# Optimization experiments

Hardware: AMD Instinct MI355X
Metric: run time of the kernel (lower is better)

The kernel has to match this reference:

```python
import jax, jax.numpy as jnp
import numpy as np

BSZ, SEQ, HID = 4, 2048, 2048
NH, NKV, HD = 16, 8, 128
SLOTS, MAXSEQ = 8, 4096
EPS = 1e-6
SCALE = HD ** -0.5


def rms_norm(x, w):
    # normalize over last dim (head_dim)
    var = jnp.mean(jnp.square(x), axis=-1, keepdims=True)
    return x * jax.lax.rsqrt(var + EPS) * w


def setup_inputs() -> dict:
    key = jax.random.key(0)
    ks = jax.random.split(key, 6)
    return {
        "hidden_states": jax.random.normal(ks[0], (BSZ, SEQ, HID), jnp.float32),
        "positions": jnp.tile(jnp.arange(SEQ, dtype=jnp.int32)[None, :], (BSZ, 1)),
        "k_cache": jnp.zeros((SLOTS, MAXSEQ, NKV, HD), jnp.float32),
        "v_cache": jnp.zeros((SLOTS, MAXSEQ, NKV, HD), jnp.float32),
        "slot_mapping": jnp.arange(BSZ, dtype=jnp.int32),
        "kv_start_indices": jnp.zeros((BSZ,), jnp.int32),
        "seq_lens": jnp.full((BSZ,), SEQ, jnp.int32),
        "qkv_w": jax.random.normal(ks[1], ((NH + 2 * NKV) * HD, HID), jnp.float32) * 0.02,
        "qkv_b": jax.random.normal(ks[2], ((NH + 2 * NKV) * HD,), jnp.float32) * 0.02,
        "o_w": jax.random.normal(ks[3], (HID, NH * HD), jnp.float32) * 0.02,
        "q_norm_w": jnp.ones((HD,), jnp.float32),
        "k_norm_w": jnp.ones((HD,), jnp.float32),
    }


def reference(hidden_states, positions, k_cache, v_cache, slot_mapping,
              kv_start_indices, seq_lens, qkv_w, qkv_b, o_w, q_norm_w, k_norm_w):
    bsz, seq_len, _ = hidden_states.shape
    qkv = jnp.einsum("bsh,oh->bso", hidden_states, qkv_w) + qkv_b
    q, k, v = jnp.split(qkv, [NH * HD, NH * HD + NKV * HD], axis=-1)
    q = rms_norm(q.reshape(bsz, seq_len, NH, HD), q_norm_w)
    k = rms_norm(k.reshape(bsz, seq_len, NKV, HD), k_norm_w)
    v = v.reshape(bsz, seq_len, NKV, HD)

    # paged KV cache scatter: cache[slot, start:start+seq] = k/v  (vectorized over batch)
    rows = kv_start_indices[:, None] + jnp.arange(seq_len)[None, :]  # [B,S]
    k_cache = k_cache.at[slot_mapping[:, None], rows].set(k)
    v_cache = v_cache.at[slot_mapping[:, None], rows].set(v)

    # prefill path (seq_len > 1): gather back up to max_l (= seq_len here, static)
    max_l = seq_len
    k_h = k_cache[slot_mapping, :max_l].transpose(0, 2, 1, 3)  # [B,Hkv,L,D]
    v_h = v_cache[slot_mapping, :max_l].transpose(0, 2, 1, 3)
    n_rep = NH // NKV
    if n_rep > 1:  # repeat_interleave over head dim (GQA)
        k_h = jnp.repeat(k_h, n_rep, axis=1)
        v_h = jnp.repeat(v_h, n_rep, axis=1)

    qh = q.transpose(0, 2, 1, 3)  # [B,H,S,D]
    scores = jnp.einsum("bhqd,bhkd->bhqk", qh, k_h) * SCALE
    causal = jnp.tril(jnp.ones((seq_len, max_l), bool))
    scores = jnp.where(causal[None, None], scores, -jnp.inf)
    attn = jax.nn.softmax(scores, axis=-1)
    out = jnp.einsum("bhqk,bhkd->bhqd", attn, v_h)
    out = out.transpose(0, 2, 1, 3).reshape(bsz, seq_len, NH * HD)
    return jnp.einsum("bso,ho->bsh", out, o_w)
```

## Files before the change

kernel.cpp:

```cpp
#include <hip/hip_runtime.h>
#include <hip/hip_bf16.h>
#include <stdint.h>

typedef unsigned short u16;
typedef __attribute__((ext_vector_type(8))) __bf16 bf16x8;
typedef __attribute__((ext_vector_type(4))) float f32x4;

#define EPSF 1e-6f
#define SCALE 0.08838834764831845f

__device__ __forceinline__ u16 f2bf(float f) {
    union { float f; uint32_t u; } a; a.f = f;
    uint32_t r = a.u + 0x7FFFu + ((a.u >> 16) & 1u);
    return (u16)(r >> 16);
}
__device__ __forceinline__ float bf2f(u16 u) {
    union { uint32_t u; float f; } a; a.u = ((uint32_t)u) << 16;
    return a.f;
}
__device__ __forceinline__ u16 f2bf_n(float f) {
    __hip_bfloat16 h = __float2bfloat16(f);
    return *reinterpret_cast<u16*>(&h);
}

__global__ __launch_bounds__(256) void cvt_all_k(
    const float* __restrict__ a,
    const float* __restrict__ b,
    const float* __restrict__ c,
    u16* __restrict__ out)
{
    long i = (long)blockIdx.x * 256 + threadIdx.x;
    const float* src; long off;
    if (i < 4194304L)      { src = a; off = 0; }
    else if (i < 6291456L) { src = b; off = 4194304L; }
    else                   { src = c; off = 6291456L; }
    float4 v = ((const float4*)src)[i - off];
    ushort4 o;
    o.x = f2bf(v.x); o.y = f2bf(v.y); o.z = f2bf(v.z); o.w = f2bf(v.w);
    ((ushort4*)out)[i] = o;
}

__device__ __forceinline__ void gload16(const u16* g, u16* l) {
    __builtin_amdgcn_global_load_lds(
        (const __attribute__((address_space(1))) uint32_t*)g,
        (__attribute__((address_space(3))) uint32_t*)l, 16, 0, 0);
}

__global__ __launch_bounds__(512, 2) void gemm8_nt(
    const u16* __restrict__ A, const u16* __restrict__ B,
    const float* __restrict__ bias,
    float* __restrict__ Cf, u16* __restrict__ Cb,
    int M, int N, int K)
{
    __shared__ u16 As[2][256 * 64];
    __shared__ u16 Bs[2][256 * 64];

    const int t = threadIdx.x;
    const int lane = t & 63;
    const int g = lane >> 4, lr = lane & 15;
    const int w = t >> 6;
    const int wm = w >> 2, wn = w & 3;

    const int nwg = gridDim.x * gridDim.y;
    const int bid0 = blockIdx.y * gridDim.x + blockIdx.x;
    const int cpx = nwg >> 3;
    const int bids = (bid0 & 7) * cpx + (bid0 >> 3);
    const int bn = (bids % gridDim.x) * 256;
    const int bm = (bids / gridDim.x) * 256;
    const int NT = K >> 6;

    f32x4 z = {0.f, 0.f, 0.f, 0.f};
    f32x4 acc[8][4];
#pragma unroll
    for (int m = 0; m < 8; ++m)
#pragma unroll
        for (int n = 0; n < 4; ++n) acc[m][n] = z;

    auto STAGE2 = [&](int buf, int k0, int p) {
#pragma unroll
        for (int j = 0; j < 2; ++j) {
            int idx = p * 1024 + j * 512 + t;
            int ci = idx & 2047;
            int row = ci >> 3, slot = ci & 7;
            int csrc = slot ^ (row & 7);
            if (idx < 2048)
                gload16(A + (size_t)(bm + row) * K + k0 + csrc * 8, &As[buf][0] + ci * 8);
            else
                gload16(B + (size_t)(bn + row) * K + k0 + csrc * 8, &Bs[buf][0] + ci * 8);
        }
    };

    bf16x8 afr0[4][2], afr1[4][2];
    bf16x8 bf0[2][2], bf1[2][2];

#pragma unroll
    for (int p = 0; p < 4; ++p) STAGE2(0, 0, p);

    for (int kt = 0; kt < NT; ++kt) {
        const int cur = kt & 1;
        const int k0n = (kt + 1) << 6;
        const bool last = (kt == NT - 1);
        const char* Ab = (const char*)&As[cur][0];
        const char* Bb = (const char*)&Bs[cur][0];
        const int swz = (lr & 7) << 4;

        auto LDA = [&](bf16x8 (&dst)[4][2], int mbase) {
#pragma unroll
            for (int mi = 0; mi < 4; ++mi) {
                int row = wm * 128 + (mbase + mi) * 16 + lr;
#pragma unroll
                for (int kc = 0; kc < 2; ++kc)
                    dst[mi][kc] = *(const bf16x8*)(Ab + row * 128 + ((kc * 64 + g * 16) ^ swz));
            }
        };
        auto LDB = [&](bf16x8 (&dst)[2][2], int nbase) {
#pragma unroll
            for (int ni = 0; ni < 2; ++ni) {
                int row = wn * 64 + (nbase + ni) * 16 + lr;
#pragma unroll
                for (int kc = 0; kc < 2; ++kc)
                    dst[ni][kc] = *(const bf16x8*)(Bb + row * 128 + ((kc * 64 + g * 16) ^ swz));
            }
        };
        auto MMA = [&](bf16x8 (&amf)[4][2], int mf0, int nf0, bf16x8 (&bfr)[2][2]) {
            __builtin_amdgcn_s_setprio(1);
#pragma unroll
            for (int mi = 0; mi < 4; ++mi)
#pragma unroll
                for (int ni = 0; ni < 2; ++ni)
#pragma unroll
                    for (int kc = 0; kc < 2; ++kc)
                        acc[mf0 + mi][nf0 + ni] = __builtin_amdgcn_mfma_f32_16x16x32_bf16(
                            amf[mi][kc], bfr[ni][kc], acc[mf0 + mi][nf0 + ni], 0, 0, 0);
            __builtin_amdgcn_s_setprio(0);
        };

        if (!last) {
#pragma unroll
            for (int p = 0; p < 4; ++p) STAGE2(cur ^ 1, k0n, p);
            asm volatile("s_waitcnt vmcnt(8)" ::: "memory");
        } else {
            asm volatile("s_waitcnt vmcnt(0)" ::: "memory");
        }
        __builtin_amdgcn_s_barrier();
        __builtin_amdgcn_sched_barrier(0);

        LDA(afr0, 0); LDB(bf0, 0); LDB(bf1, 2);
        MMA(afr0, 0, 0, bf0);
        MMA(afr0, 0, 2, bf1);
        LDA(afr1, 4);
        MMA(afr1, 4, 2, bf1);
        MMA(afr1, 4, 0, bf0);

        __builtin_amdgcn_sched_barrier(0);
        __builtin_amdgcn_s_barrier();
    }

#pragma unroll
    for (int mf = 0; mf < 8; ++mf) {
#pragma unroll
        for (int nf = 0; nf < 4; ++nf) {
            int col = bn + wn * 64 + nf * 16 + lr;
            float bv = bias ? bias[col] : 0.f;
#pragma unroll
            for (int r = 0; r < 4; ++r) {
                int row = bm + wm * 128 + mf * 16 + g * 4 + r;
                float v = acc[mf][nf][r] + bv;
                if (Cf) Cf[(size_t)row * N + col] = v;
                else    Cb[(size_t)row * N + col] = f2bf(v);
            }
        }
    }
}

__global__ __launch_bounds__(256) void prep_k(
    u16* __restrict__ qkv, const float* __restrict__ qw, const float* __restrict__ kw,
    u16* __restrict__ vt)
{
    __shared__ u16 T[64 * 64];
    const int bid = blockIdx.x;
    const int t = threadIdx.x;

    if (bid < 8192) {
        const int row = bid;
        const int w = t >> 6, l = t & 63;
#pragma unroll
        for (int i = 0; i < 6; ++i) {
            int head = w + i * 4;
            const float* wt = (head < 16) ? qw : kw;
            u16* p = qkv + (size_t)row * 4096 + head * 128;
            uint32_t u = *(const uint32_t*)(p + l * 2);
            float x0 = bf2f((u16)(u & 0xFFFF));
            float x1 = bf2f((u16)(u >> 16));
            float ss = x0 * x0 + x1 * x1;
#pragma unroll
            for (int m = 1; m < 64; m <<= 1) ss += __shfl_xor(ss, m, 64);
            float inv = rsqrtf(ss * (1.0f / 128.0f) + EPSF);
            float r0 = x0 * inv * wt[l * 2];
            float r1 = x1 * inv * wt[l * 2 + 1];
            uint32_t o = (uint32_t)f2bf(r0) | ((uint32_t)f2bf(r1) << 16);
            *(uint32_t*)(p + l * 2) = o;
        }
    } else {
        const int q = bid - 8192;
        const int sx = (q & 31) * 64;
        const int dy = ((q >> 5) & 1) * 64;
        const int z  = q >> 6;
        const int b = z >> 3, hk = z & 7;
#pragma unroll
        for (int j = 0; j < 2; ++j) {
            int idx = t + j * 256;
            int r = idx >> 3, c8 = (idx & 7) * 8;
            uint4 v = *(const uint4*)(qkv + (size_t)(b * 2048 + sx + r) * 4096 + 3072 + hk * 128 + dy + c8);
            int slot = (c8 >> 3) ^ ((r ^ (r >> 3)) & 7);
            *(uint4*)(&T[r * 64 + slot * 8]) = v;
        }
        __syncthreads();
#pragma unroll
        for (int j = 0; j < 2; ++j) {
            int idx = t + j * 256;
            int rr = idx >> 3, cc8 = (idx & 7) * 8;
            u16 tmp[8];
#pragma unroll
            for (int i = 0; i < 8; ++i) {
                int row = cc8 + i;
                int slot = (rr >> 3) ^ ((row ^ (row >> 3)) & 7);
                tmp[i] = T[row * 64 + slot * 8 + (rr & 7)];
            }
            *(uint4*)(vt + ((size_t)z * 128 + dy + rr) * 2048 + sx + cc8) = *(uint4*)tmp;
        }
    }
}

#define P_S 72

__global__ __launch_bounds__(256, 2) void attn5_k(
    const u16* __restrict__ qkv, const u16* __restrict__ vt,
    u16* __restrict__ aout)
{
    __shared__ u16 Kt[2][64 * 128];
    __shared__ u16 Vl[2][128 * 64];
    __shared__ u16 P[4][16 * P_S];

    const int t = threadIdx.x;
    const int lane = t & 63;
    const int w = t >> 6;
    const int g = lane >> 4, lr = lane & 15;
    const int pr = blockIdx.x, h = blockIdx.y, b = blockIdx.z;
    const int hk = h >> 1;
    const size_t rowb = (size_t)b * 2048;

    const u16* ksrc = qkv + rowb * 4096 + 2048 + hk * 128;
    const u16* vsrc = vt + (size_t)(b * 8 + hk) * 128 * 2048;

    bf16x8 ones8;
    {
        union { bf16x8 v; u16 e[8]; } on;
#pragma unroll
        for (int j = 0; j < 8; ++j) on.e[j] = 0x3F80;
        ones8 = on.v;
    }

    auto STAGE = [&](int buf, int kvb) {
#pragma unroll
        for (int j = 0; j < 4; ++j) {
            int idx = t + j * 256;
            {
                int row = idx >> 4, slot = idx & 15;
                int csrc = (slot & 8) | ((slot & 7) ^ (row & 7));
                gload16(ksrc + (size_t)(kvb + row) * 4096 + csrc * 8, &Kt[buf][0] + idx * 8);
            }
            {
                int row = idx >> 3, slot = idx & 7;
                int csrc = slot ^ (row & 7);
                gload16(vsrc + (size_t)row * 2048 + kvb + csrc * 8, &Vl[buf][0] + idx * 8);
            }
        }
    };

    for (int sub = 0; sub < 2; ++sub) {
        const int qt = sub ? 15 - pr : pr;
        const int qbase = qt * 128;
        const int nt = 2 * qt + 2;

        bf16x8 qf[2][4];
        {
            const u16* qp = qkv + (rowb + qbase + w * 32 + lr) * 4096 + h * 128;
#pragma unroll
            for (int sb = 0; sb < 2; ++sb)
#pragma unroll
                for (int c = 0; c < 4; ++c) {
                    union { bf16x8 v; u16 e[8]; } uq;
                    uq.v = *(const bf16x8*)(qp + sb * 16 * 4096 + c * 32 + g * 8);
#pragma unroll
                    for (int jj = 0; jj < 8; ++jj) uq.e[jj] = f2bf(bf2f(uq.e[jj]) * SCALE);
                    qf[sb][c] = uq.v;
                }
        }

        float m_r[2][4];
        f32x4 z = {0.f, 0.f, 0.f, 0.f};
        f32x4 l_acc[2];
        f32x4 o_acc[2][8];
#pragma unroll
        for (int sb = 0; sb < 2; ++sb) {
#pragma unroll
            for (int r = 0; r < 4; ++r) m_r[sb][r] = -INFINITY;
            l_acc[sb] = z;
#pragma unroll
            for (int d = 0; d < 8; ++d) o_acc[sb][d] = z;
        }

        __syncthreads();
        STAGE(0, 0);

        for (int kt = 0; kt < nt; ++kt) {
            const int cur = kt & 1;
            const int kvb = kt * 64;
            asm volatile("s_waitcnt vmcnt(0)" ::: "memory");
            __builtin_amdgcn_s_barrier();
            __builtin_amdgcn_sched_barrier(0);
            if (kt + 1 < nt) STAGE(cur ^ 1, kvb + 64);
            __builtin_amdgcn_sched_barrier(0);

            const u16* Kc = &Kt[cur][0];
            const u16* Vc = &Vl[cur][0];
            const bool active = !(kt == nt - 1 && w < 2);
            const bool near = (kt >= nt - 2);

            if (active) {
                f32x4 s[2][4];
                __builtin_amdgcn_s_setprio(1);
#pragma unroll
                for (int cb = 0; cb < 4; ++cb) {
                    int row = cb * 16 + lr;
                    s[0][cb] = z; s[1][cb] = z;
#pragma unroll
                    for (int c = 0; c < 4; ++c) {
                        int chunk = c * 4 + g;
                        int slot = (chunk & 8) | ((chunk & 7) ^ (row & 7));
                        bf16x8 kf = *(const bf16x8*)(&Kc[row * 128 + slot * 8]);
                        s[0][cb] = __builtin_amdgcn_mfma_f32_16x16x32_bf16(qf[0][c], kf, s[0][cb], 0, 0, 0);
                        s[1][cb] = __builtin_amdgcn_mfma_f32_16x16x32_bf16(qf[1][c], kf, s[1][cb], 0, 0, 0);
                    }
                }
                __builtin_amdgcn_s_setprio(0);

#pragma unroll
                for (int sb = 0; sb < 2; ++sb) {
#pragma unroll
                    for (int r = 0; r < 4; ++r) {
                        float v0 = s[sb][0][r], v1 = s[sb][1][r], v2 = s[sb][2][r], v3 = s[sb][3][r];
                        if (near) {
                            int qa = qbase + w * 32 + sb * 16 + g * 4 + r;
                            if (kvb + lr > qa)      v0 = -INFINITY;
                            if (kvb + 16 + lr > qa) v1 = -INFINITY;
                            if (kvb + 32 + lr > qa) v2 = -INFINITY;
                            if (kvb + 48 + lr > qa) v3 = -INFINITY;
                        }
                        float mx = fmaxf(fmaxf(v0, v1), fmaxf(v2, v3));
                        mx = fmaxf(mx, __shfl_xor(mx, 1));
                        mx = fmaxf(mx, __shfl_xor(mx, 2));
                        mx = fmaxf(mx, __shfl_xor(mx, 4));
                        mx = fmaxf(mx, __shfl_xor(mx, 8));
                        float mold = m_r[sb][r];
                        float mbase;
                        if (__all(mx <= mold + 8.0f)) {
                            mbase = mold;
                        } else {
                            float mnew = fmaxf(mold, mx);
                            float alpha = __expf(mold - mnew);
                            l_acc[sb][r] *= alpha;
#pragma unroll
                            for (int d = 0; d < 8; ++d) o_acc[sb][d][r] *= alpha;
                            m_r[sb][r] = mnew;
                            mbase = mnew;
                        }
                        float p0 = __expf(v0 - mbase), p1 = __expf(v1 - mbase);
                        float p2 = __expf(v2 - mbase), p3 = __expf(v3 - mbase);
                        int prow = (g * 4 + r) * P_S;
                        P[w][prow + lr]      = f2bf_n(p0);
                        P[w][prow + 16 + lr] = f2bf_n(p1);
                        P[w][prow + 32 + lr] = f2bf_n(p2);
                        P[w][prow + 48 + lr] = f2bf_n(p3);
                    }

#pragma unroll
                    for (int kk = 0; kk < 2; ++kk) {
                        bf16x8 pa = *(const bf16x8*)(&P[w][lr * P_S + kk * 32 + g * 8]);
                        __builtin_amdgcn_s_setprio(1);
                        l_acc[sb] = __builtin_amdgcn_mfma_f32_16x16x32_bf16(pa, ones8, l_acc[sb], 0, 0, 0);
#pragma unroll
                        for (int d = 0; d < 8; ++d) {
                            int row = d * 16 + lr;
                            int slot = (kk * 4 + g) ^ (row & 7);
                            bf16x8 vf = *(const bf16x8*)(&Vc[row * 64 + slot * 8]);
                            o_acc[sb][d] = __builtin_amdgcn_mfma_f32_16x16x32_bf16(pa, vf, o_acc[sb][d], 0, 0, 0);
                        }
                        __builtin_amdgcn_s_setprio(0);
                    }
                }
            }
            __builtin_amdgcn_sched_barrier(0);
        }

#pragma unroll
        for (int sb = 0; sb < 2; ++sb) {
            const int qrow0 = qbase + w * 32 + sb * 16 + g * 4;
#pragma unroll
            for (int r = 0; r < 4; ++r) {
                float inv = 1.0f / l_acc[sb][r];
                u16* op = aout + (rowb + qrow0 + r) * 2048 + h * 128;
#pragma unroll
                for (int d = 0; d < 8; ++d)
                    op[d * 16 + lr] = f2bf_n(o_acc[sb][d][r] * inv);
            }
        }
    }
}

extern "C" void kernel_launch(void* const* d_in, const int* in_sizes, int n_in,
                              void* d_out, int out_size, void* d_ws, size_t ws_size,
                              hipStream_t stream)
{
    const float* hidden = (const float*)d_in[0];
    const float* qkv_w = (const float*)d_in[7];
    const float* qkv_b = (const float*)d_in[8];
    const float* o_w   = (const float*)d_in[9];
    const float* q_nw  = (const float*)d_in[10];
    const float* k_nw  = (const float*)d_in[11];

    char* ws = (char*)d_ws;
    u16* hid_bf  = (u16*)ws; ws += (size_t)8192 * 2048 * 2;
    u16* wqkv_bf = (u16*)ws; ws += (size_t)4096 * 2048 * 2;
    u16* ow_bf   = (u16*)ws; ws += (size_t)2048 * 2048 * 2;
    u16* qkv_bf  = (u16*)ws; ws += (size_t)8192 * 4096 * 2;
    u16* attn_bf = (u16*)ws; ws += (size_t)8192 * 2048 * 2;
    u16* vt_bf   = hid_bf;

    cvt_all_k<<<28672, 256, 0, stream>>>(hidden, qkv_w, o_w, hid_bf);

    gemm8_nt<<<dim3(16, 32), 512, 0, stream>>>(hid_bf, wqkv_bf, qkv_b,
                                               nullptr, qkv_bf, 8192, 4096, 2048);
    prep_k<<<dim3(10240), 256, 0, stream>>>(qkv_bf, q_nw, k_nw, vt_bf);
    attn5_k<<<dim3(8, 16, 4), 256, 0, stream>>>(qkv_bf, vt_bf, attn_bf);
    gemm8_nt<<<dim3(8, 32), 512, 0, stream>>>(attn_bf, ow_bf, nullptr,
                                              (float*)d_out, nullptr, 8192, 2048, 2048);
}
```

Measured before the change: 404.1 us.

## Compute transposed scores and pass softmax probabilities via lane shuffles instead of LDS

The QK^T MFMA operands are swapped, so each lane holds score columns for a single query row. The row max then needs only two cross-lane shuffles, and each lane keeps one running max per row block instead of four. Probabilities are packed to bf16 in registers and redistributed into the PV MFMA operand layout with __shfl, which removes the per-wave LDS P buffer and its store/load round trip. In exchange the kernel issues more ds_bpermute shuffles and select instructions, and rescaling needs an extra shuffle to broadcast alpha to each row.

Result: faster. 378.1 us (median of 2 runs) (-6.4%).

```diff
diff --git a/kernel.cpp b/kernel.cpp
--- a/kernel.cpp
+++ b/kernel.cpp
@@ -232,15 +232,12 @@
     }
 }
 
-#define P_S 72
-
-__global__ __launch_bounds__(256, 2) void attn5_k(
+__global__ __launch_bounds__(256, 2) void attn7_k(
     const u16* __restrict__ qkv, const u16* __restrict__ vt,
     u16* __restrict__ aout)
 {
     __shared__ u16 Kt[2][64 * 128];
     __shared__ u16 Vl[2][128 * 64];
-    __shared__ u16 P[4][16 * P_S];
 
     const int t = threadIdx.x;
     const int lane = t & 63;
@@ -298,14 +295,13 @@
                 }
         }
 
-        float m_r[2][4];
+        float m_r2[2];
         f32x4 z = {0.f, 0.f, 0.f, 0.f};
         f32x4 l_acc[2];
         f32x4 o_acc[2][8];
 #pragma unroll
         for (int sb = 0; sb < 2; ++sb) {
-#pragma unroll
-            for (int r = 0; r < 4; ++r) m_r[sb][r] = -INFINITY;
+            m_r2[sb] = -INFINITY;
             l_acc[sb] = z;
 #pragma unroll
             for (int d = 0; d < 8; ++d) o_acc[sb][d] = z;
@@ -329,73 +325,96 @@
             const bool near = (kt >= nt - 2);
 
             if (active) {
-                f32x4 s[2][4];
+                f32x4 st[2][4];
                 __builtin_amdgcn_s_setprio(1);
 #pragma unroll
                 for (int cb = 0; cb < 4; ++cb) {
                     int row = cb * 16 + lr;
-                    s[0][cb] = z; s[1][cb] = z;
+                    st[0][cb] = z; st[1][cb] = z;
 #pragma unroll
                     for (int c = 0; c < 4; ++c) {
                         int chunk = c * 4 + g;
                         int slot = (chunk & 8) | ((chunk & 7) ^ (row & 7));
                         bf16x8 kf = *(const bf16x8*)(&Kc[row * 128 + slot * 8]);
-                        s[0][cb] = __builtin_amdgcn_mfma_f32_16x16x32_bf16(qf[0][c], kf, s[0][cb], 0, 0, 0);
-                        s[1][cb] = __builtin_amdgcn_mfma_f32_16x16x32_bf16(qf[1][c], kf, s[1][cb], 0, 0, 0);
+                        st[0][cb] = __builtin_amdgcn_mfma_f32_16x16x32_bf16(kf, qf[0][c], st[0][cb], 0, 0, 0);
+                        st[1][cb] = __builtin_amdgcn_mfma_f32_16x16x32_bf16(kf, qf[1][c], st[1][cb], 0, 0, 0);
                     }
                 }
                 __builtin_amdgcn_s_setprio(0);
 
+                const int slo = ((g & 1) << 5) + lr;
+                const int shi = slo + 16;
+                const bool ghx = (g >> 1) & 1;
+
 #pragma unroll
                 for (int sb = 0; sb < 2; ++sb) {
-#pragma unroll
-                    for (int r = 0; r < 4; ++r) {
-                        float v0 = s[sb][0][r], v1 = s[sb][1][r], v2 = s[sb][2][r], v3 = s[sb][3][r];
-                        if (near) {
-                            int qa = qbase + w * 32 + sb * 16 + g * 4 + r;
-                            if (kvb + lr > qa)      v0 = -INFINITY;
-                            if (kvb + 16 + lr > qa) v1 = -INFINITY;
-                            if (kvb + 32 + lr > qa) v2 = -INFINITY;
-                            if (kvb + 48 + lr > qa) v3 = -INFINITY;
+                    const int qa = qbase + w * 32 + sb * 16 + lr;
+                    if (near) {
+#pragma unroll
+                        for (int cb = 0; cb < 4; ++cb)
+#pragma unroll
+                            for (int r = 0; r < 4; ++r)
+                                if (kvb + cb * 16 + g * 4 + r > qa) st[sb][cb][r] = -INFINITY;
+                    }
+                    f32x4 m4;
+#pragma unroll
+                    for (int e = 0; e < 4; ++e)
+                        m4[e] = fmaxf(fmaxf(st[sb][0][e], st[sb][1][e]),
+                                      fmaxf(st[sb][2][e], st[sb][3][e]));
+                    float mx = fmaxf(fmaxf(m4[0], m4[1]), fmaxf(m4[2], m4[3]));
+                    mx = fmaxf(mx, __shfl_xor(mx, 16));
+                    mx = fmaxf(mx, __shfl_xor(mx, 32));
+                    float mold = m_r2[sb];
+                    float mbase;
+                    if (__all(mx <= mold + 8.0f)) {
+                        mbase = mold;
+                    } else {
+                        float mnew = fmaxf(mold, mx);
+                        float alpha = __expf(mold - mnew);
+#pragma unroll
+                        for (int r = 0; r < 4; ++r) {
+                            float ar = __shfl(alpha, (lane & 48) | (g * 4 + r), 64);
+                            l_acc[sb][r] *= ar;
+#pragma unroll
+                            for (int d = 0; d < 8; ++d) o_acc[sb][d][r] *= ar;
                         }
-                        float mx = fmaxf(fmaxf(v0, v1), fmaxf(v2, v3));
-                        mx = fmaxf(mx, __shfl_xor(mx, 1));
-                        mx = fmaxf(mx, __shfl_xor(mx, 2));
-                        mx = fmaxf(mx, __shfl_xor(mx, 4));
-                        mx = fmaxf(mx, __shfl_xor(mx, 8));
-                        float mold = m_r[sb][r];
-                        float mbase;
-                        if (__all(mx <= mold + 8.0f)) {
-                            mbase = mold;
-                        } else {
-                            float mnew = fmaxf(mold, mx);
-                            float alpha = __expf(mold - mnew);
-                            l_acc[sb][r] *= alpha;
-#pragma unroll
-                            for (int d = 0; d < 8; ++d) o_acc[sb][d][r] *= alpha;
-                            m_r[sb][r] = mnew;
-                            mbase = mnew;
-                        }
-                        float p0 = __expf(v0 - mbase), p1 = __expf(v1 - mbase);
-                        float p2 = __expf(v2 - mbase), p3 = __expf(v3 - mbase);
-                        int prow = (g * 4 + r) * P_S;
-                        P[w][prow + lr]      = f2bf_n(p0);
-                        P[w][prow + 16 + lr] = f2bf_n(p1);
-                        P[w][prow + 32 + lr] = f2bf_n(p2);
-                        P[w][prow + 48 + lr] = f2bf_n(p3);
+                        m_r2[sb] = mnew;
+                        mbase = mnew;
                     }
+                    uint2 pk[4];
+#pragma unroll
+                    for (int cb = 0; cb < 4; ++cb) {
+                        float p0 = __expf(st[sb][cb][0] - mbase);
+                        float p1 = __expf(st[sb][cb][1] - mbase);
+                        float p2 = __expf(st[sb][cb][2] - mbase);
+                        float p3 = __expf(st[sb][cb][3] - mbase);
+                        pk[cb].x = (uint32_t)f2bf_n(p0) | ((uint32_t)f2bf_n(p1) << 16);
+                        pk[cb].y = (uint32_t)f2bf_n(p2) | ((uint32_t)f2bf_n(p3) << 16);
+                    }
 
 #pragma unroll
                     for (int kk = 0; kk < 2; ++kk) {
-                        bf16x8 pa = *(const bf16x8*)(&P[w][lr * P_S + kk * 32 + g * 8]);
+                        uint32_t e0 = (uint32_t)__shfl((int)pk[kk * 2].x, slo, 64);
+                        uint32_t e1 = (uint32_t)__shfl((int)pk[kk * 2].y, slo, 64);
+                        uint32_t e2 = (uint32_t)__shfl((int)pk[kk * 2].x, shi, 64);
+                        uint32_t e3 = (uint32_t)__shfl((int)pk[kk * 2].y, shi, 64);
+                        uint32_t o0 = (uint32_t)__shfl((int)pk[kk * 2 + 1].x, slo, 64);
+                        uint32_t o1 = (uint32_t)__shfl((int)pk[kk * 2 + 1].y, slo, 64);
+                        uint32_t o2 = (uint32_t)__shfl((int)pk[kk * 2 + 1].x, shi, 64);
+                        uint32_t o3 = (uint32_t)__shfl((int)pk[kk * 2 + 1].y, shi, 64);
+                        union { uint32_t u[4]; bf16x8 v; } pa;
+                        pa.u[0] = ghx ? o0 : e0;
+                        pa.u[1] = ghx ? o1 : e1;
+                        pa.u[2] = ghx ? o2 : e2;
+                        pa.u[3] = ghx ? o3 : e3;
                         __builtin_amdgcn_s_setprio(1);
-                        l_acc[sb] = __builtin_amdgcn_mfma_f32_16x16x32_bf16(pa, ones8, l_acc[sb], 0, 0, 0);
+                        l_acc[sb] = __builtin_amdgcn_mfma_f32_16x16x32_bf16(pa.v, ones8, l_acc[sb], 0, 0, 0);
 #pragma unroll
                         for (int d = 0; d < 8; ++d) {
                             int row = d * 16 + lr;
                             int slot = (kk * 4 + g) ^ (row & 7);
                             bf16x8 vf = *(const bf16x8*)(&Vc[row * 64 + slot * 8]);
-                            o_acc[sb][d] = __builtin_amdgcn_mfma_f32_16x16x32_bf16(pa, vf, o_acc[sb][d], 0, 0, 0);
+                            o_acc[sb][d] = __builtin_amdgcn_mfma_f32_16x16x32_bf16(pa.v, vf, o_acc[sb][d], 0, 0, 0);
                         }
                         __builtin_amdgcn_s_setprio(0);
                     }
@@ -443,7 +462,7 @@
     gemm8_nt<<<dim3(16, 32), 512, 0, stream>>>(hid_bf, wqkv_bf, qkv_b,
                                                nullptr, qkv_bf, 8192, 4096, 2048);
     prep_k<<<dim3(10240), 256, 0, stream>>>(qkv_bf, q_nw, k_nw, vt_bf);
-    attn5_k<<<dim3(8, 16, 4), 256, 0, stream>>>(qkv_bf, vt_bf, attn_bf);
+    attn7_k<<<dim3(8, 16, 4), 256, 0, stream>>>(qkv_bf, vt_bf, attn_bf);
     gemm8_nt<<<dim3(8, 32), 512, 0, stream>>>(attn_bf, ow_bf, nullptr,
                                               (float*)d_out, nullptr, 8192, 2048, 2048);
 }
```
